# Kernel optimization log

Measured on AMD Instinct MI355X. Metric: run time of the kernel, lower is better.

## Reference

```python
import jax, jax.numpy as jnp
import numpy as np

NUM_TREE = 64
TREE_DEPTH = 4
NUM_LEAF = 2 ** (TREE_DEPTH + 1)        # 32
NUM_INTERNALS = NUM_LEAF - 1            # 31
IN_DIM = 512
OUT_DIM = 16
BATCH = 8192


def build_route_masks(tree_depth: int, num_internals: int, num_leaf: int) -> np.ndarray:
    """Static gather indices into the [p, 1-p] concatenated prob vector (length 2*num_internals).
    Returns [tree_depth+1, num_leaf]; product over level axis gives leaf path probabilities.
    Mirrors the increment_mask construction in the torch forward."""
    masks = []
    num_repeat = num_leaf // 2
    num_local_internals = 1
    masks.append(np.repeat(np.array([0, num_internals]), num_repeat))
    for _ in range(1, tree_depth + 1):
        num_repeat //= 2
        num_local_internals *= 2
        m = np.repeat(np.arange(num_local_internals - 1, 2 * num_local_internals - 1), 2)
        m = m + np.tile(np.array([0, num_internals]), num_local_internals)
        m = np.repeat(m, num_repeat)
        masks.append(m)
    return np.stack(masks).astype(np.int32)  # [depth+1, num_leaf]


ROUTE_MASKS = jnp.asarray(build_route_masks(TREE_DEPTH, NUM_INTERNALS, NUM_LEAF))


def setup_inputs() -> dict:
    key = jax.random.key(0)
    k1, k2, k3 = jax.random.split(key, 3)
    x = jax.random.normal(k1, (BATCH, IN_DIM), dtype=jnp.float32)
    # xavier-ish scale so sigmoid gates are not saturated
    W = jax.random.normal(k2, (NUM_TREE * NUM_INTERNALS, IN_DIM), dtype=jnp.float32) / np.sqrt(IN_DIM)
    b = jnp.zeros((NUM_TREE * NUM_INTERNALS,), dtype=jnp.float32)
    leafs = jax.random.normal(k3, (NUM_TREE, NUM_LEAF, OUT_DIM), dtype=jnp.float32)
    return {"x": x, "W": W, "b": b, "leafs": leafs}


def reference(x, W, b, leafs) -> jnp.ndarray:
    B = x.shape[0]
    T, L, O = leafs.shape
    I = L - 1
    tree_net = x @ W.T + b                                  # [B, T*I]
    p = jax.nn.sigmoid(tree_net).reshape(B, T, I)           # split per tree
    flat = jnp.concatenate([p, 1.0 - p], axis=-1)           # [B, T, 2I]
    gathered = flat[:, :, ROUTE_MASKS]                      # [B, T, depth+1, L]
    routes = jnp.prod(gathered, axis=2)                     # [B, T, L] leaf path probs
    leafs_sm = jax.nn.softmax(leafs, axis=-1)
    features = routes.reshape(B, T * L)
    out = features @ leafs_sm.reshape(T * L, O) / T
    return out
```

## Files before the change

kernel.cpp:

```cpp
#include <hip/hip_runtime.h>

#define BATCH 8192
#define IN_DIM 512
#define NT 64
#define NI 31
#define NL 32
#define ODIM 16
#define NPAD (NT*NL)
#define NCB 16

typedef __attribute__((ext_vector_type(8))) short bf16x8;
typedef __attribute__((ext_vector_type(4))) float f32x4;

__device__ __forceinline__ unsigned short f2b(float f) {
  union { float f; unsigned int u; } v; v.f = f;
  unsigned int r = v.u + 0x7fffu + ((v.u >> 16) & 1u);
  return (unsigned short)(r >> 16);
}
__device__ __forceinline__ float b2f(unsigned short h) {
  union { unsigned int u; float f; } v; v.u = ((unsigned int)h) << 16;
  return v.f;
}

__global__ __launch_bounds__(256) void prep_kernel(
    const float* __restrict__ x, const float* __restrict__ W,
    const float* __restrict__ leafs,
    unsigned short* __restrict__ xb, unsigned short* __restrict__ wb,
    float* __restrict__ lsm)
{
  const int NXg = BATCH * (IN_DIM/8);
  const int NWg = NPAD  * (IN_DIM/8);
  const int NS  = NT*NL;
  int gid = blockIdx.x*256 + threadIdx.x;
  if (gid < NXg) {
    int row = gid >> 6, k8 = gid & 63;
    int kt = k8 >> 2, g = k8 & 3;
    int gs = g ^ ((row >> 1) & 3);
    const float* s = x + (size_t)row*IN_DIM + kt*32 + gs*8;
    float4 v0 = ((const float4*)s)[0], v1 = ((const float4*)s)[1];
    ushort4 o0, o1;
    o0.x=f2b(v0.x); o0.y=f2b(v0.y); o0.z=f2b(v0.z); o0.w=f2b(v0.w);
    o1.x=f2b(v1.x); o1.y=f2b(v1.y); o1.z=f2b(v1.z); o1.w=f2b(v1.w);
    ((ushort4*)xb)[gid*2]   = o0;
    ((ushort4*)xb)[gid*2+1] = o1;
  } else if ((gid -= NXg) < NWg) {
    int row = gid >> 6, k8 = gid & 63;
    int t = row >> 5, i = row & 31;
    int kt = k8 >> 2, g = k8 & 3;
    int gs = g ^ ((row >> 1) & 3);
    ushort4 o0, o1;
    if (i == 31) { o0.x=o0.y=o0.z=o0.w=0; o1=o0; }
    else {
      const float* s = W + (size_t)(t*NI+i)*IN_DIM + kt*32 + gs*8;
      float4 v0 = ((const float4*)s)[0], v1 = ((const float4*)s)[1];
      o0.x=f2b(v0.x); o0.y=f2b(v0.y); o0.z=f2b(v0.z); o0.w=f2b(v0.w);
      o1.x=f2b(v1.x); o1.y=f2b(v1.y); o1.z=f2b(v1.z); o1.w=f2b(v1.w);
    }
    ((ushort4*)wb)[gid*2]   = o0;
    ((ushort4*)wb)[gid*2+1] = o1;
  } else if ((gid -= NWg) < NS) {
    const float* src = leafs + (size_t)gid*ODIM;
    float m = src[0];
    #pragma unroll
    for (int o=1;o<ODIM;++o) m = fmaxf(m, src[o]);
    float e[ODIM]; float s = 0.f;
    #pragma unroll
    for (int o=0;o<ODIM;++o) { e[o] = __expf(src[o]-m); s += e[o]; }
    float inv = 1.f/(s*(float)NT);
    #pragma unroll
    for (int o=0;o<ODIM;++o) lsm[(size_t)gid*ODIM+o] = e[o]*inv;
  }
}

__device__ __forceinline__ void async16(const unsigned short* g, unsigned short* l) {
  __builtin_amdgcn_global_load_lds(
      (const __attribute__((address_space(1))) unsigned int*)g,
      (__attribute__((address_space(3))) unsigned int*)l,
      16, 0, 0);
}

#define STG 12288

__global__ __launch_bounds__(256, 2) void fused_kernel(
    const unsigned short* __restrict__ xb, const unsigned short* __restrict__ wb,
    const float* __restrict__ bias, const float* __restrict__ lsm,
    float* __restrict__ part)
{
  __shared__ __align__(16) unsigned short smem[36864];

  const int tid  = threadIdx.x;
  const int lane = tid & 63;
  const int wave = tid >> 6;
  const int wm = wave & 1, wn = wave >> 1;

  const int bid = blockIdx.x;
  const int m_t = (bid & 7)*4 + (bid >> 7);
  const int n_t = (bid >> 3) & 15;
  const int m0 = m_t * 256, n0 = n_t * 128;

  f32x4 acc[8][4];
  #pragma unroll
  for (int i=0;i<8;++i)
    #pragma unroll
    for (int j=0;j<4;++j) { f32x4 z = {0.f,0.f,0.f,0.f}; acc[i][j] = z; }

  const int srow = lane >> 2, scol = (lane & 3) * 8;
  const unsigned short* gaw = xb + (size_t)(m0 + wave*64 + srow)*IN_DIM + scol;
  const unsigned short* gbw = wb + (size_t)(n0 + wave*32 + srow)*IN_DIM + scol;

  const int l15 = lane & 15, quad = lane >> 4;
  const int cs   = (quad ^ ((l15 >> 1) & 3)) << 3;

  #pragma unroll
  for (int c=0;c<4;++c) async16(gaw + c*16*IN_DIM,      smem + wave*2048 + c*512);
  #pragma unroll
  for (int c=0;c<2;++c) async16(gbw + c*16*IN_DIM,      smem + 8192 + wave*1024 + c*512);
  #pragma unroll
  for (int c=0;c<4;++c) async16(gaw + 32 + c*16*IN_DIM, smem + STG + wave*2048 + c*512);
  #pragma unroll
  for (int c=0;c<2;++c) async16(gbw + 32 + c*16*IN_DIM, smem + STG + 8192 + wave*1024 + c*512);

  unsigned short* st0 = smem;
  unsigned short* st1 = smem + STG;
  unsigned short* st2 = smem + 2*STG;

  for (int kt = 0; kt < 15; ++kt) {
    asm volatile("s_waitcnt vmcnt(6)" ::: "memory");
    __builtin_amdgcn_s_barrier();
    if (kt < 14) {
      const int ko = (kt + 2) * 32;
      #pragma unroll
      for (int c=0;c<4;++c)
        async16(gaw + ko + c*16*IN_DIM, st2 + wave*2048 + c*512);
      #pragma unroll
      for (int c=0;c<2;++c)
        async16(gbw + ko + c*16*IN_DIM, st2 + 8192 + wave*1024 + c*512);
    }
    const unsigned short* As = st0;
    const unsigned short* Bs = st0 + 8192;
    bf16x8 af[8], bfr[4];
    #pragma unroll
    for (int mi=0;mi<8;++mi)
      af[mi] = *(const bf16x8*)(As + (wm*128 + mi*16 + l15)*32 + cs);
    #pragma unroll
    for (int ni=0;ni<4;++ni)
      bfr[ni] = *(const bf16x8*)(Bs + (wn*64 + ni*16 + l15)*32 + cs);
    __builtin_amdgcn_s_setprio(1);
    #pragma unroll
    for (int mi=0;mi<8;++mi)
      #pragma unroll
      for (int ni=0;ni<4;++ni)
        acc[mi][ni] = __builtin_amdgcn_mfma_f32_16x16x32_bf16(
            af[mi], bfr[ni], acc[mi][ni], 0, 0, 0);
    __builtin_amdgcn_s_setprio(0);
    unsigned short* t = st0; st0 = st1; st1 = st2; st2 = t;
  }
  asm volatile("s_waitcnt vmcnt(0)" ::: "memory");
  __builtin_amdgcn_s_barrier();
  {
    const unsigned short* As = st0;
    const unsigned short* Bs = st0 + 8192;
    bf16x8 af[8], bfr[4];
    #pragma unroll
    for (int mi=0;mi<8;++mi)
      af[mi] = *(const bf16x8*)(As + (wm*128 + mi*16 + l15)*32 + cs);
    #pragma unroll
    for (int ni=0;ni<4;++ni)
      bfr[ni] = *(const bf16x8*)(Bs + (wn*64 + ni*16 + l15)*32 + cs);
    __builtin_amdgcn_s_setprio(1);
    #pragma unroll
    for (int mi=0;mi<8;++mi)
      #pragma unroll
      for (int ni=0;ni<4;++ni)
        acc[mi][ni] = __builtin_amdgcn_mfma_f32_16x16x32_bf16(
            af[mi], bfr[ni], acc[mi][ni], 0, 0, 0);
    __builtin_amdgcn_s_setprio(0);
  }

  bf16x8 bleaf[4];
  {
    const int t0 = n_t * 4;
    #pragma unroll
    for (int s=0;s<4;++s) {
      union { bf16x8 v; unsigned short u[8]; } tmp;
      #pragma unroll
      for (int j=0;j<8;++j)
        tmp.u[j] = f2b(lsm[((size_t)(t0+s)*NL + quad*8 + j)*ODIM + l15]);
      bleaf[s] = tmp.v;
    }
  }

  __syncthreads();

  unsigned short* Pt = smem;
  #pragma unroll
  for (int ni=0;ni<4;++ni) {
    int cl = wn*64 + ni*16 + l15;
    int gcol = n0 + cl;
    int tt = gcol >> 5, ii = gcol & 31;
    float bv = (ii < NI) ? bias[tt*NI + ii] : 0.f;
    #pragma unroll
    for (int mi=0;mi<8;++mi) {
      int lrow = wm*128 + mi*16 + quad*4;
      #pragma unroll
      for (int r=0;r<4;++r) {
        float v = acc[mi][ni][r] + bv;
        Pt[(lrow + r)*132 + cl] = f2b(1.f/(1.f + __expf(-v)));
      }
    }
  }
  __syncthreads();

  const int row = tid;
  unsigned int rt[64];
  #pragma unroll
  for (int tl=0; tl<4; ++tl) {
    const short4* pr4 = (const short4*)(Pt + row*132 + tl*32);
    union { short4 v4[8]; unsigned short u[32]; } qb;
    #pragma unroll
    for (int c=0;c<8;++c) qb.v4[c] = pr4[c];
    float q[31];
    #pragma unroll
    for (int i=0;i<31;++i) q[i] = b2f(qb.u[i]);
    float v[32];
    v[0] = q[0]; v[1] = 1.f - q[0];
    #pragma unroll
    for (int d=1; d<=4; ++d) {
      const int s = 1 << d;
      #pragma unroll
      for (int j=s-1; j>=0; --j) {
        float pj = q[(s-1)+j];
        float base = v[j];
        v[2*j]   = base * pj;
        v[2*j+1] = base * (1.f - pj);
      }
    }
    #pragma unroll
    for (int k=0;k<16;++k)
      rt[tl*16+k] = (unsigned int)f2b(v[2*k]) | ((unsigned int)f2b(v[2*k+1]) << 16);
  }
  __syncthreads();

  unsigned int* Rt32 = (unsigned int*)smem;
  {
    uint4* dst = (uint4*)(Rt32 + row*68);
    #pragma unroll
    for (int c=0;c<16;++c) {
      uint4 w; w.x=rt[c*4]; w.y=rt[c*4+1]; w.z=rt[c*4+2]; w.w=rt[c*4+3];
      dst[c] = w;
    }
  }
  __syncthreads();

  const unsigned short* RtS = smem;
  #pragma unroll
  for (int mt=0; mt<4; ++mt) {
    const int mrow = (wave*4 + mt)*16;
    f32x4 a2 = {0.f,0.f,0.f,0.f};
    #pragma unroll
    for (int s=0;s<4;++s) {
      bf16x8 af2 = *(const bf16x8*)(RtS + (mrow + l15)*136 + s*32 + quad*8);
      a2 = __builtin_amdgcn_mfma_f32_16x16x32_bf16(af2, bleaf[s], a2, 0, 0, 0);
    }
    float* op = part + ((size_t)n_t*BATCH + (m0 + mrow + quad*4))*ODIM + l15;
    #pragma unroll
    for (int r=0;r<4;++r)
      op[r*ODIM] = a2[r];
  }
}

__global__ __launch_bounds__(256) void reduce_kernel(
    const float* __restrict__ part, float* __restrict__ out)
{
  int gid = blockIdx.x*256 + threadIdx.x;
  const float4* p4 = (const float4*)part;
  float4 s = p4[gid];
  #pragma unroll
  for (int cb=1; cb<NCB; ++cb) {
    float4 v = p4[(size_t)cb*(BATCH*ODIM/4) + gid];
    s.x+=v.x; s.y+=v.y; s.z+=v.z; s.w+=v.w;
  }
  ((float4*)out)[gid] = s;
}

extern "C" void kernel_launch(void* const* d_in, const int* in_sizes, int n_in,
                              void* d_out, int out_size, void* d_ws, size_t ws_size,
                              hipStream_t stream) {
  const float* x     = (const float*)d_in[0];
  const float* W     = (const float*)d_in[1];
  const float* b     = (const float*)d_in[2];
  const float* leafs = (const float*)d_in[3];
  float* out = (float*)d_out;

  char* ws = (char*)d_ws;
  unsigned short* xb  = (unsigned short*)ws;
  unsigned short* wb  = (unsigned short*)(ws + 8388608);
  float*          lsm = (float*)(ws + 10485760);
  float*          part= (float*)(ws + 10616832);

  const int total = BATCH*(IN_DIM/8) + NPAD*(IN_DIM/8) + NT*NL;
  prep_kernel<<<dim3((total + 255)/256), dim3(256), 0, stream>>>(
      x, W, leafs, xb, wb, lsm);
  fused_kernel<<<dim3(512), dim3(256), 0, stream>>>(
      xb, wb, b, lsm, part);
  reduce_kernel<<<dim3(BATCH*ODIM/4/256), dim3(256), 0, stream>>>(part, out);
}
```

Baseline: 103.4 us.

## Fuse prep and GEMM into cooperative kernel with atomic output reduction

Merges the prep, GEMM and reduce launches into one cooperative mega-kernel. The prep work runs as a grid-stride phase that also zeroes the output, followed by a grid-wide sync and then the GEMM phase. The GEMM phase accumulates into the output with atomicAdd instead of writing per-column-block partials for a separate reduce kernel. This removes launch overhead and the partials round trip, at the cost of a grid barrier, atomic contention on 16 column blocks per output, and float-summation order that is no longer deterministic. A two-kernel fallback runs if the cooperative launch fails.

```diff
diff --git a/kernel.cpp b/kernel.cpp
--- a/kernel.cpp
+++ b/kernel.cpp
@@ -1,4 +1,7 @@
 #include <hip/hip_runtime.h>
+#include <hip/hip_cooperative_groups.h>
+
+namespace cg = cooperative_groups;
 
 #define BATCH 8192
 #define IN_DIM 512
@@ -7,7 +10,6 @@
 #define NL 32
 #define ODIM 16
 #define NPAD (NT*NL)
-#define NCB 16
 
 typedef __attribute__((ext_vector_type(8))) short bf16x8;
 typedef __attribute__((ext_vector_type(4))) float f32x4;
@@ -20,56 +22,6 @@
 __device__ __forceinline__ float b2f(unsigned short h) {
   union { unsigned int u; float f; } v; v.u = ((unsigned int)h) << 16;
   return v.f;
-}
-
-__global__ __launch_bounds__(256) void prep_kernel(
-    const float* __restrict__ x, const float* __restrict__ W,
-    const float* __restrict__ leafs,
-    unsigned short* __restrict__ xb, unsigned short* __restrict__ wb,
-    float* __restrict__ lsm)
-{
-  const int NXg = BATCH * (IN_DIM/8);
-  const int NWg = NPAD  * (IN_DIM/8);
-  const int NS  = NT*NL;
-  int gid = blockIdx.x*256 + threadIdx.x;
-  if (gid < NXg) {
-    int row = gid >> 6, k8 = gid & 63;
-    int kt = k8 >> 2, g = k8 & 3;
-    int gs = g ^ ((row >> 1) & 3);
-    const float* s = x + (size_t)row*IN_DIM + kt*32 + gs*8;
-    float4 v0 = ((const float4*)s)[0], v1 = ((const float4*)s)[1];
-    ushort4 o0, o1;
-    o0.x=f2b(v0.x); o0.y=f2b(v0.y); o0.z=f2b(v0.z); o0.w=f2b(v0.w);
-    o1.x=f2b(v1.x); o1.y=f2b(v1.y); o1.z=f2b(v1.z); o1.w=f2b(v1.w);
-    ((ushort4*)xb)[gid*2]   = o0;
-    ((ushort4*)xb)[gid*2+1] = o1;
-  } else if ((gid -= NXg) < NWg) {
-    int row = gid >> 6, k8 = gid & 63;
-    int t = row >> 5, i = row & 31;
-    int kt = k8 >> 2, g = k8 & 3;
-    int gs = g ^ ((row >> 1) & 3);
-    ushort4 o0, o1;
-    if (i == 31) { o0.x=o0.y=o0.z=o0.w=0; o1=o0; }
-    else {
-      const float* s = W + (size_t)(t*NI+i)*IN_DIM + kt*32 + gs*8;
-      float4 v0 = ((const float4*)s)[0], v1 = ((const float4*)s)[1];
-      o0.x=f2b(v0.x); o0.y=f2b(v0.y); o0.z=f2b(v0.z); o0.w=f2b(v0.w);
-      o1.x=f2b(v1.x); o1.y=f2b(v1.y); o1.z=f2b(v1.z); o1.w=f2b(v1.w);
-    }
-    ((ushort4*)wb)[gid*2]   = o0;
-    ((ushort4*)wb)[gid*2+1] = o1;
-  } else if ((gid -= NWg) < NS) {
-    const float* src = leafs + (size_t)gid*ODIM;
-    float m = src[0];
-    #pragma unroll
-    for (int o=1;o<ODIM;++o) m = fmaxf(m, src[o]);
-    float e[ODIM]; float s = 0.f;
-    #pragma unroll
-    for (int o=0;o<ODIM;++o) { e[o] = __expf(src[o]-m); s += e[o]; }
-    float inv = 1.f/(s*(float)NT);
-    #pragma unroll
-    for (int o=0;o<ODIM;++o) lsm[(size_t)gid*ODIM+o] = e[o]*inv;
-  }
 }
 
 __device__ __forceinline__ void async16(const unsigned short* g, unsigned short* l) {
@@ -81,13 +33,70 @@
 
 #define STG 12288
 
-__global__ __launch_bounds__(256, 2) void fused_kernel(
+__device__ void phaseP(
+    const float* __restrict__ x, const float* __restrict__ W,
+    const float* __restrict__ leafs,
+    unsigned short* __restrict__ xb, unsigned short* __restrict__ wb,
+    float* __restrict__ lsm, float* __restrict__ out)
+{
+  const int NXg = BATCH * (IN_DIM/8);
+  const int NWg = NPAD  * (IN_DIM/8);
+  const int NS  = NT*NL;
+  const int NZ  = BATCH*ODIM/4;
+  const int TOTALP = NXg + NWg + NS + NZ;
+  const int stride = gridDim.x * 256;
+  for (int task = blockIdx.x*256 + threadIdx.x; task < TOTALP; task += stride) {
+    int gid = task;
+    if (gid < NXg) {
+      int row = gid >> 6, k8 = gid & 63;
+      int kt = k8 >> 2, g = k8 & 3;
+      int gs = g ^ ((row >> 1) & 3);
+      const float* s = x + (size_t)row*IN_DIM + kt*32 + gs*8;
+      float4 v0 = ((const float4*)s)[0], v1 = ((const float4*)s)[1];
+      ushort4 o0, o1;
+      o0.x=f2b(v0.x); o0.y=f2b(v0.y); o0.z=f2b(v0.z); o0.w=f2b(v0.w);
+      o1.x=f2b(v1.x); o1.y=f2b(v1.y); o1.z=f2b(v1.z); o1.w=f2b(v1.w);
+      ((ushort4*)xb)[gid*2]   = o0;
+      ((ushort4*)xb)[gid*2+1] = o1;
+    } else if ((gid -= NXg) < NWg) {
+      int row = gid >> 6, k8 = gid & 63;
+      int t = row >> 5, i = row & 31;
+      int kt = k8 >> 2, g = k8 & 3;
+      int gs = g ^ ((row >> 1) & 3);
+      ushort4 o0, o1;
+      if (i == 31) { o0.x=o0.y=o0.z=o0.w=0; o1=o0; }
+      else {
+        const float* s = W + (size_t)(t*NI+i)*IN_DIM + kt*32 + gs*8;
+        float4 v0 = ((const float4*)s)[0], v1 = ((const float4*)s)[1];
+        o0.x=f2b(v0.x); o0.y=f2b(v0.y); o0.z=f2b(v0.z); o0.w=f2b(v0.w);
+        o1.x=f2b(v1.x); o1.y=f2b(v1.y); o1.z=f2b(v1.z); o1.w=f2b(v1.w);
+      }
+      ((ushort4*)wb)[gid*2]   = o0;
+      ((ushort4*)wb)[gid*2+1] = o1;
+    } else if ((gid -= NWg) < NS) {
+      const float* src = leafs + (size_t)gid*ODIM;
+      float m = src[0];
+      #pragma unroll
+      for (int o=1;o<ODIM;++o) m = fmaxf(m, src[o]);
+      float e[ODIM]; float s = 0.f;
+      #pragma unroll
+      for (int o=0;o<ODIM;++o) { e[o] = __expf(src[o]-m); s += e[o]; }
+      float inv = 1.f/(s*(float)NT);
+      #pragma unroll
+      for (int o=0;o<ODIM;++o) lsm[(size_t)gid*ODIM+o] = e[o]*inv;
+    } else {
+      int z = gid - NS;
+      float4 zero = {0.f,0.f,0.f,0.f};
+      ((float4*)out)[z] = zero;
+    }
+  }
+}
+
+__device__ void phaseG(
     const unsigned short* __restrict__ xb, const unsigned short* __restrict__ wb,
     const float* __restrict__ bias, const float* __restrict__ lsm,
-    float* __restrict__ part)
-{
-  __shared__ __align__(16) unsigned short smem[36864];
-
+    float* __restrict__ out, unsigned short* smem)
+{
   const int tid  = threadIdx.x;
   const int lane = tid & 63;
   const int wave = tid >> 6;
@@ -262,25 +271,41 @@
       bf16x8 af2 = *(const bf16x8*)(RtS + (mrow + l15)*136 + s*32 + quad*8);
       a2 = __builtin_amdgcn_mfma_f32_16x16x32_bf16(af2, bleaf[s], a2, 0, 0, 0);
     }
-    float* op = part + ((size_t)n_t*BATCH + (m0 + mrow + quad*4))*ODIM + l15;
+    float* op = out + (size_t)(m0 + mrow + quad*4)*ODIM + l15;
     #pragma unroll
     for (int r=0;r<4;++r)
-      op[r*ODIM] = a2[r];
-  }
-}
-
-__global__ __launch_bounds__(256) void reduce_kernel(
-    const float* __restrict__ part, float* __restrict__ out)
-{
-  int gid = blockIdx.x*256 + threadIdx.x;
-  const float4* p4 = (const float4*)part;
-  float4 s = p4[gid];
-  #pragma unroll
-  for (int cb=1; cb<NCB; ++cb) {
-    float4 v = p4[(size_t)cb*(BATCH*ODIM/4) + gid];
-    s.x+=v.x; s.y+=v.y; s.z+=v.z; s.w+=v.w;
-  }
-  ((float4*)out)[gid] = s;
+      atomicAdd(op + r*ODIM, a2[r]);
+  }
+}
+
+__global__ __launch_bounds__(256, 2) void mega_kernel(
+    const float* __restrict__ x, const float* __restrict__ W,
+    const float* __restrict__ bias, const float* __restrict__ leafs,
+    unsigned short* __restrict__ xb, unsigned short* __restrict__ wb,
+    float* __restrict__ lsm, float* __restrict__ out)
+{
+  __shared__ __align__(16) unsigned short smem[36864];
+  phaseP(x, W, leafs, xb, wb, lsm, out);
+  cg::this_grid().sync();
+  phaseG(xb, wb, bias, lsm, out, smem);
+}
+
+__global__ __launch_bounds__(256) void prep_kernel(
+    const float* __restrict__ x, const float* __restrict__ W,
+    const float* __restrict__ leafs,
+    unsigned short* __restrict__ xb, unsigned short* __restrict__ wb,
+    float* __restrict__ lsm, float* __restrict__ out)
+{
+  phaseP(x, W, leafs, xb, wb, lsm, out);
+}
+
+__global__ __launch_bounds__(256, 2) void gemm_kernel(
+    const unsigned short* __restrict__ xb, const unsigned short* __restrict__ wb,
+    const float* __restrict__ bias, const float* __restrict__ lsm,
+    float* __restrict__ out)
+{
+  __shared__ __align__(16) unsigned short smem[36864];
+  phaseG(xb, wb, bias, lsm, out, smem);
 }
 
 extern "C" void kernel_launch(void* const* d_in, const int* in_sizes, int n_in,
@@ -296,12 +321,13 @@
   unsigned short* xb  = (unsigned short*)ws;
   unsigned short* wb  = (unsigned short*)(ws + 8388608);
   float*          lsm = (float*)(ws + 10485760);
-  float*          part= (float*)(ws + 10616832);
-
-  const int total = BATCH*(IN_DIM/8) + NPAD*(IN_DIM/8) + NT*NL;
-  prep_kernel<<<dim3((total + 255)/256), dim3(256), 0, stream>>>(
-      x, W, leafs, xb, wb, lsm);
-  fused_kernel<<<dim3(512), dim3(256), 0, stream>>>(
-      xb, wb, b, lsm, part);
-  reduce_kernel<<<dim3(BATCH*ODIM/4/256), dim3(256), 0, stream>>>(part, out);
-}
+
+  void* args[] = { (void*)&x, (void*)&W, (void*)&b, (void*)&leafs,
+                   (void*)&xb, (void*)&wb, (void*)&lsm, (void*)&out };
+  hipError_t e = hipLaunchCooperativeKernel(
+      (const void*)mega_kernel, dim3(512), dim3(256), args, 0, stream);
+  if (e != hipSuccess) {
+    prep_kernel<<<dim3(512), dim3(256), 0, stream>>>(x, W, leafs, xb, wb, lsm, out);
+    gemm_kernel<<<dim3(512), dim3(256), 0, stream>>>(xb, wb, b, lsm, out);
+  }
+}
```

Measured after the change: 174.9 us. 69.2% more time.
